# Performance work log

Hardware: AMD Instinct MI355X
Metric: run time of the kernel (lower is better)

Reference implementation:

```python
import jax, jax.numpy as jnp
import numpy as np

N_NODES = 100000
N_EDGES = 1600000
D = 64
K1 = 10   # conv1 hops
K2 = 3    # stacked conv hops


def _gcn_norm(edge_index, num_nodes, dtype):
    # PyG gcn_norm with add_self_loops=False: sym normalization D^-1/2 A D^-1/2
    row, col = edge_index[0], edge_index[1]
    deg = jax.ops.segment_sum(jnp.ones(row.shape, dtype), col, num_segments=num_nodes)
    dinv = jnp.where(deg > 0, jax.lax.rsqrt(jnp.maximum(deg, 1.0)), 0.0)
    return dinv[row] * dinv[col]  # [E]


def _tagconv(x, ws, b, row, col, nrm, num_nodes):
    # out = sum_k (A_hat^k x) @ W_k + b ; ws: [K+1, D, D]
    out = x @ ws[0]
    h = x
    for k in range(1, ws.shape[0]):
        msg = h[row] * nrm[:, None]                       # [E, D] gather
        h = jax.ops.segment_sum(msg, col, num_segments=num_nodes)  # [N, D] scatter-add
        out = out + h @ ws[k]
    return out + b


def setup_inputs() -> dict:
    key = jax.random.key(0)
    ks = jax.random.split(key, 8)
    x = jax.random.normal(ks[0], (N_NODES, D), dtype=jnp.float32)
    edge_index = jax.random.randint(ks[1], (2, N_EDGES), 0, N_NODES, dtype=jnp.int64)
    s = 1.0 / np.sqrt(D)
    w1 = jax.random.normal(ks[2], (K1 + 1, D, D), dtype=jnp.float32) * s
    b1 = jnp.zeros((D,), dtype=jnp.float32)
    w2 = jax.random.normal(ks[3], (K2 + 1, D, D), dtype=jnp.float32) * s
    b2 = jnp.zeros((D,), dtype=jnp.float32)
    wc = jax.random.normal(ks[4], (D, D), dtype=jnp.float32) * s
    bc = jnp.zeros((D,), dtype=jnp.float32)
    return {"x": x, "edge_index": edge_index, "w1": w1, "b1": b1,
            "w2": w2, "b2": b2, "wc": wc, "bc": bc}


def reference(x, edge_index, w1, b1, w2, b2, wc, bc):
    num_nodes = x.shape[0]
    row, col = edge_index[0], edge_index[1]
    nrm = _gcn_norm(edge_index, num_nodes, x.dtype)
    h = jnp.tanh(_tagconv(x, w1, b1, row, col, nrm, num_nodes))
    h = jnp.tanh(_tagconv(h, w2, b2, row, col, nrm, num_nodes))
    return h @ wc + bc
```

## Files before the change

kernel.cpp:

```cpp
#include <hip/hip_runtime.h>
#include <hip/hip_bf16.h>

#define PAD 16
#define NBKT_MAX 512

typedef __attribute__((ext_vector_type(8))) short short8;
typedef __attribute__((ext_vector_type(4))) float float4v;

__device__ __forceinline__ short8 as_s8(uint4 v) {
    union { uint4 u; short8 s; } x; x.u = v; return x.s;
}


__global__ void deg_kernel(const int* __restrict__ col, int* __restrict__ deg, int E) {
    int e = blockIdx.x * blockDim.x + threadIdx.x;
    if (e < E) atomicAdd(&deg[col[e]], 1);
}

__global__ void dinv_kernel(const int* __restrict__ deg, float* __restrict__ dinv,
                            float* __restrict__ dinv2, float* __restrict__ sdeg, int N) {
    int n = blockIdx.x * blockDim.x + threadIdx.x;
    if (n < N) {
        int d = deg[n];
        float v = d > 0 ? rsqrtf((float)d) : 0.0f;
        dinv[n] = v;
        dinv2[n] = v * v;
        sdeg[n] = d > 0 ? sqrtf((float)d) : 0.0f;
    }
}

__device__ __forceinline__ int pad_up(int v) { return (v + (PAD - 1)) & ~(PAD - 1); }

__global__ void scan_phaseA(const int* __restrict__ deg, int* __restrict__ chunkSum, int N) {
    int t = threadIdx.x;
    int idx = blockIdx.x * 512 + t;
    int v = idx < N ? pad_up(deg[idx]) : 0;
    for (int o = 32; o > 0; o >>= 1) v += __shfl_down(v, o, 64);
    __shared__ int wsum[8];
    if ((t & 63) == 0) wsum[t >> 6] = v;
    __syncthreads();
    if (t == 0) {
        int s = 0;
        for (int i = 0; i < 8; ++i) s += wsum[i];
        chunkSum[blockIdx.x] = s;
    }
}

__global__ void scan_phaseB(const int* __restrict__ in, int* __restrict__ outp, int n) {
    __shared__ int a[256], b[256];
    int t = threadIdx.x;
    int v = t < n ? in[t] : 0;
    a[t] = v;
    __syncthreads();
    int* s = a; int* d = b;
    for (int off = 1; off < 256; off <<= 1) {
        int x = s[t];
        if (t >= off) x += s[t - off];
        d[t] = x;
        __syncthreads();
        int* tmp = s; s = d; d = tmp;
    }
    if (t < n) outp[t] = s[t] - v;
}

__global__ void scan_phaseC(const int* __restrict__ deg, const int* __restrict__ chunkOff,
                            int* __restrict__ rowptr, int N) {
    __shared__ int a[512], b[512];
    int t = threadIdx.x;
    int idx = blockIdx.x * 512 + t;
    int v = idx < N ? pad_up(deg[idx]) : 0;
    a[t] = v;
    __syncthreads();
    int* s = a; int* d = b;
    for (int off = 1; off < 512; off <<= 1) {
        int x = s[t];
        if (t >= off) x += s[t - off];
        d[t] = x;
        __syncthreads();
        int* tmp = s; s = d; d = tmp;
    }
    if (idx < N) rowptr[idx] = chunkOff[blockIdx.x] + s[t] - v;
    if (idx == N - 1) rowptr[N] = chunkOff[blockIdx.x] + s[t];
}


__global__ __launch_bounds__(256) void hist_kernel(const int* __restrict__ col,
                                                   int* __restrict__ blockHist, int E, int nbkt) {
    __shared__ int h[NBKT_MAX];
    for (int i = threadIdx.x; i < nbkt; i += 256) h[i] = 0;
    __syncthreads();
    int chunk = (E + gridDim.x - 1) / gridDim.x;
    int lo = blockIdx.x * chunk, hi = min(lo + chunk, E);
    for (int e = lo + threadIdx.x; e < hi; e += 256) atomicAdd(&h[col[e] >> 9], 1);
    __syncthreads();
    for (int i = threadIdx.x; i < nbkt; i += 256) blockHist[i * 256 + blockIdx.x] = h[i];
}

__global__ __launch_bounds__(256) void bscan_kernel(int* __restrict__ blockHist,
                                                    int* __restrict__ bktTot, int nbkt) {
    __shared__ int a[256], b[256];
    int bkt = blockIdx.x;
    int t = threadIdx.x;
    int v = blockHist[bkt * 256 + t];
    a[t] = v;
    __syncthreads();
    int* s = a; int* d = b;
    for (int off = 1; off < 256; off <<= 1) {
        int x = s[t];
        if (t >= off) x += s[t - off];
        d[t] = x;
        __syncthreads();
        int* tmp = s; s = d; d = tmp;
    }
    blockHist[bkt * 256 + t] = s[t] - v;
    if (t == 255) bktTot[bkt] = s[t];
}

__global__ __launch_bounds__(256) void scatter_kernel(const int* __restrict__ row,
                                                      const int* __restrict__ col,
                                                      const int* __restrict__ blockHist,
                                                      const int* __restrict__ bktOff,
                                                      int2* __restrict__ pairs, int E, int nbkt) {
    __shared__ int cur[NBKT_MAX];
    for (int i = threadIdx.x; i < nbkt; i += 256)
        cur[i] = bktOff[i] + blockHist[i * 256 + blockIdx.x];
    __syncthreads();
    int chunk = (E + gridDim.x - 1) / gridDim.x;
    int lo = blockIdx.x * chunk, hi = min(lo + chunk, E);
    for (int e = lo + threadIdx.x; e < hi; e += 256) {
        int dn = col[e];
        int p = atomicAdd(&cur[dn >> 9], 1);
        pairs[p] = make_int2(row[e], dn);
    }
}

__global__ __launch_bounds__(256) void cluster_kernel(const int2* __restrict__ pairs,
                                                      const int* __restrict__ bktOff,
                                                      const int* __restrict__ bktTot,
                                                      const int* __restrict__ rowptr,
                                                      int* __restrict__ srcs, int N) {
    __shared__ int cur[512];
    int b = blockIdx.x;
    int d0 = b << 9;
    for (int i = threadIdx.x; i < 512; i += 256) {
        int d = d0 + i;
        cur[i] = (d < N) ? rowptr[d] : 0;
    }
    __syncthreads();
    int lo = bktOff[b], hi = lo + bktTot[b];
    for (int p = lo + threadIdx.x; p < hi; p += 256) {
        int2 e = pairs[p];
        int pos = atomicAdd(&cur[e.y - d0], 1);
        srcs[pos] = e.x;
    }
}

__global__ void pad_kernel(const int* __restrict__ deg, const int* __restrict__ rowptr,
                           int* __restrict__ srcs, int N) {
    int dn = blockIdx.x * blockDim.x + threadIdx.x;
    if (dn < N) {
        int p = rowptr[dn] + deg[dn];
        int p1 = rowptr[dn + 1];
        for (; p < p1; ++p) srcs[p] = N;
    }
}

__global__ void wcvt_kernel(const float* __restrict__ w1, const float* __restrict__ w2,
                            const float* __restrict__ wc, __hip_bfloat16* __restrict__ wf) {
    int idx = blockIdx.x * blockDim.x + threadIdx.x;
    if (idx >= 16 * 4096) return;
    int g = idx >> 12, r = idx & 4095;
    int j = r & 7, lane = (r >> 3) & 63, u = (r >> 9) & 3, t = r >> 11;
    int k = t * 32 + (lane >> 4) * 8 + j;
    int n = u * 16 + (lane & 15);
    const float* W = (g < 11) ? (w1 + (size_t)g * 4096)
                  : (g < 15) ? (w2 + (size_t)(g - 11) * 4096) : wc;
    wf[idx] = __float2bfloat16(W[k * 64 + n]);
}

__global__ void zero_pads_kernel(__hip_bfloat16* __restrict__ gbase, size_t gstride,
                                 int nbuf, int N) {
    int i = blockIdx.x * blockDim.x + threadIdx.x;
    int b = i >> 6;
    if (b < nbuf) gbase[(size_t)b * gstride + (size_t)N * 64 + (i & 63)] = __float2bfloat16(0.0f);
}

__global__ void cvt_g_kernel(const float* __restrict__ x, const float* __restrict__ dinv,
                             __hip_bfloat16* __restrict__ g, int N) {
    int i = blockIdx.x * blockDim.x + threadIdx.x;
    if (i < N * 64) g[i] = __float2bfloat16(dinv[i >> 6] * x[i]);
}


__global__ __launch_bounds__(256) void hop_kernel(
        const __hip_bfloat16* __restrict__ g_in,
        const int* __restrict__ srcs, const int* __restrict__ rowptr,
        const float* __restrict__ dinv2,
        __hip_bfloat16* __restrict__ g_out, int n) {
    const int lane = threadIdx.x & 63;
    int gw = __builtin_amdgcn_readfirstlane((blockIdx.x * blockDim.x + threadIdx.x) >> 6);
    int nw = (gridDim.x * blockDim.x) >> 6;
    for (int d = gw; d < n; d += nw) {
        int p0 = rowptr[d], p1 = rowptr[d + 1];
        float agg = 0.f;
        for (int p = p0; p < p1; p += 16) {
            int s0  = srcs[p + 0],  s1  = srcs[p + 1],  s2  = srcs[p + 2],  s3  = srcs[p + 3];
            int s4  = srcs[p + 4],  s5  = srcs[p + 5],  s6  = srcs[p + 6],  s7  = srcs[p + 7];
            int s8  = srcs[p + 8],  s9  = srcs[p + 9],  s10 = srcs[p + 10], s11 = srcs[p + 11];
            int s12 = srcs[p + 12], s13 = srcs[p + 13], s14 = srcs[p + 14], s15 = srcs[p + 15];
            float v0  = __bfloat162float(g_in[(size_t)s0  * 64 + lane]);
            float v1  = __bfloat162float(g_in[(size_t)s1  * 64 + lane]);
            float v2  = __bfloat162float(g_in[(size_t)s2  * 64 + lane]);
            float v3  = __bfloat162float(g_in[(size_t)s3  * 64 + lane]);
            float v4  = __bfloat162float(g_in[(size_t)s4  * 64 + lane]);
            float v5  = __bfloat162float(g_in[(size_t)s5  * 64 + lane]);
            float v6  = __bfloat162float(g_in[(size_t)s6  * 64 + lane]);
            float v7  = __bfloat162float(g_in[(size_t)s7  * 64 + lane]);
            float v8  = __bfloat162float(g_in[(size_t)s8  * 64 + lane]);
            float v9  = __bfloat162float(g_in[(size_t)s9  * 64 + lane]);
            float v10 = __bfloat162float(g_in[(size_t)s10 * 64 + lane]);
            float v11 = __bfloat162float(g_in[(size_t)s11 * 64 + lane]);
            float v12 = __bfloat162float(g_in[(size_t)s12 * 64 + lane]);
            float v13 = __bfloat162float(g_in[(size_t)s13 * 64 + lane]);
            float v14 = __bfloat162float(g_in[(size_t)s14 * 64 + lane]);
            float v15 = __bfloat162float(g_in[(size_t)s15 * 64 + lane]);
            agg += v0;  agg += v1;  agg += v2;  agg += v3;
            agg += v4;  agg += v5;  agg += v6;  agg += v7;
            agg += v8;  agg += v9;  agg += v10; agg += v11;
            agg += v12; agg += v13; agg += v14; agg += v15;
        }
        g_out[(size_t)d * 64 + lane] = __float2bfloat16(dinv2[d] * agg);
    }
}


__global__ __launch_bounds__(256) void final_kernel(
        const __hip_bfloat16* gbase, size_t gstride, int ngemm,
        const __hip_bfloat16* __restrict__ wf,
        const float* __restrict__ sdeg, const float* __restrict__ bias,
        const float* __restrict__ scale,
        __hip_bfloat16* out16, int ntiles) {
    const int lane = threadIdx.x & 63;
    const int col = lane & 15, quad = lane >> 4;
    int wv = (blockIdx.x * blockDim.x + threadIdx.x) >> 6;
    int nwv = (gridDim.x * blockDim.x) >> 6;
    const uint4* wfq = (const uint4*)wf;
    for (int tile = wv; tile < ntiles; tile += nwv) {
        int base = tile * 16;
        float4v acc0 = {0.f, 0.f, 0.f, 0.f};
        float4v acc1 = {0.f, 0.f, 0.f, 0.f};
        float4v acc2 = {0.f, 0.f, 0.f, 0.f};
        float4v acc3 = {0.f, 0.f, 0.f, 0.f};
        for (int g = 0; g < ngemm; ++g) {
            const uint4* ga = (const uint4*)(gbase + (size_t)g * gstride);
            const uint4* wg = wfq + (size_t)g * 512;
#pragma unroll
            for (int t = 0; t < 2; ++t) {
                short8 a = as_s8(ga[(size_t)(base + col) * 8 + t * 4 + quad]);
                short8 b0 = as_s8(wg[(t * 4 + 0) * 64 + lane]);
                short8 b1 = as_s8(wg[(t * 4 + 1) * 64 + lane]);
                short8 b2 = as_s8(wg[(t * 4 + 2) * 64 + lane]);
                short8 b3 = as_s8(wg[(t * 4 + 3) * 64 + lane]);
                acc0 = __builtin_amdgcn_mfma_f32_16x16x32_bf16(a, b0, acc0, 0, 0, 0);
                acc1 = __builtin_amdgcn_mfma_f32_16x16x32_bf16(a, b1, acc1, 0, 0, 0);
                acc2 = __builtin_amdgcn_mfma_f32_16x16x32_bf16(a, b2, acc2, 0, 0, 0);
                acc3 = __builtin_amdgcn_mfma_f32_16x16x32_bf16(a, b3, acc3, 0, 0, 0);
            }
        }
#pragma unroll
        for (int r = 0; r < 4; ++r) {
            int nd = base + quad * 4 + r;
            float sd = sdeg[nd];
            float sc = scale ? scale[nd] : 1.0f;
            float f0 = sc * tanhf(sd * acc0[r] + bias[0 * 16 + col]);
            float f1 = sc * tanhf(sd * acc1[r] + bias[1 * 16 + col]);
            float f2 = sc * tanhf(sd * acc2[r] + bias[2 * 16 + col]);
            float f3 = sc * tanhf(sd * acc3[r] + bias[3 * 16 + col]);
            out16[(size_t)nd * 64 + 0 * 16 + col] = __float2bfloat16(f0);
            out16[(size_t)nd * 64 + 1 * 16 + col] = __float2bfloat16(f1);
            out16[(size_t)nd * 64 + 2 * 16 + col] = __float2bfloat16(f2);
            out16[(size_t)nd * 64 + 3 * 16 + col] = __float2bfloat16(f3);
        }
    }
}


__global__ __launch_bounds__(256) void head_kernel(
        const __hip_bfloat16* __restrict__ v16, const __hip_bfloat16* __restrict__ wfc,
        const float* __restrict__ bc, float* __restrict__ out, int ntiles) {
    const int lane = threadIdx.x & 63;
    const int col = lane & 15, quad = lane >> 4;
    int wv = (blockIdx.x * blockDim.x + threadIdx.x) >> 6;
    int nwv = (gridDim.x * blockDim.x) >> 6;
    const uint4* va = (const uint4*)v16;
    const uint4* wg = (const uint4*)wfc;
    for (int tile = wv; tile < ntiles; tile += nwv) {
        int base = tile * 16;
        float4v acc0 = {0.f, 0.f, 0.f, 0.f};
        float4v acc1 = {0.f, 0.f, 0.f, 0.f};
        float4v acc2 = {0.f, 0.f, 0.f, 0.f};
        float4v acc3 = {0.f, 0.f, 0.f, 0.f};
#pragma unroll
        for (int t = 0; t < 2; ++t) {
            short8 a = as_s8(va[(size_t)(base + col) * 8 + t * 4 + quad]);
            short8 b0 = as_s8(wg[(t * 4 + 0) * 64 + lane]);
            short8 b1 = as_s8(wg[(t * 4 + 1) * 64 + lane]);
            short8 b2 = as_s8(wg[(t * 4 + 2) * 64 + lane]);
            short8 b3 = as_s8(wg[(t * 4 + 3) * 64 + lane]);
            acc0 = __builtin_amdgcn_mfma_f32_16x16x32_bf16(a, b0, acc0, 0, 0, 0);
            acc1 = __builtin_amdgcn_mfma_f32_16x16x32_bf16(a, b1, acc1, 0, 0, 0);
            acc2 = __builtin_amdgcn_mfma_f32_16x16x32_bf16(a, b2, acc2, 0, 0, 0);
            acc3 = __builtin_amdgcn_mfma_f32_16x16x32_bf16(a, b3, acc3, 0, 0, 0);
        }
#pragma unroll
        for (int r = 0; r < 4; ++r) {
            int nd = base + quad * 4 + r;
            out[(size_t)nd * 64 + 0 * 16 + col] = acc0[r] + bc[0 * 16 + col];
            out[(size_t)nd * 64 + 1 * 16 + col] = acc1[r] + bc[1 * 16 + col];
            out[(size_t)nd * 64 + 2 * 16 + col] = acc2[r] + bc[2 * 16 + col];
            out[(size_t)nd * 64 + 3 * 16 + col] = acc3[r] + bc[3 * 16 + col];
        }
    }
}


extern "C" void kernel_launch(void* const* d_in, const int* in_sizes, int n_in,
                              void* d_out, int out_size, void* d_ws, size_t ws_size,
                              hipStream_t stream) {
    const float* x  = (const float*)d_in[0];
    const int*   ei = (const int*)d_in[1];
    const float* w1 = (const float*)d_in[2];
    const float* b1 = (const float*)d_in[3];
    const float* w2 = (const float*)d_in[4];
    const float* b2 = (const float*)d_in[5];
    const float* wc = (const float*)d_in[6];
    const float* bc = (const float*)d_in[7];
    float* out = (float*)d_out;

    const int N = in_sizes[0] / 64;
    const int E = in_sizes[1] / 2;
    const int K1 = 10, K2 = 3;
    const int* row = ei;
    const int* col = ei + E;
    const int Epad = E + (PAD - 1) * N + 64;
    const int NBUF = 11;
    const int nbkt = (N + 511) >> 9;
    const size_t gstride = (((size_t)(N + 1) * 64) + 127) & ~(size_t)127;

    char* base = (char*)d_ws;
    auto alloc = [&](size_t bytes) { void* p = (void*)base; base += (bytes + 255) & ~(size_t)255; return p; };
    int*   deg      = (int*)alloc((size_t)N * 4);
    int*   rowptr   = (int*)alloc((size_t)(N + 1) * 4);
    int*   chunkSum = (int*)alloc(256 * 4);
    int*   chunkOff = (int*)alloc(256 * 4);
    int*   blockHist= (int*)alloc((size_t)NBKT_MAX * 256 * 4);
    int*   bktTot   = (int*)alloc((size_t)NBKT_MAX * 4);
    int*   bktOff   = (int*)alloc((size_t)NBKT_MAX * 4);
    float* dinv     = (float*)alloc((size_t)N * 4);
    float* dinv2    = (float*)alloc((size_t)N * 4);
    float* sdeg     = (float*)alloc((size_t)N * 4);
    int*   srcs     = (int*)alloc((size_t)Epad * 4);
    __hip_bfloat16* wf    = (__hip_bfloat16*)alloc((size_t)16 * 4096 * 2);
    __hip_bfloat16* gbase = (__hip_bfloat16*)alloc((size_t)NBUF * gstride * 2);

    auto G = [&](int k) { return gbase + (size_t)k * gstride; };
    int2* pairs = (int2*)G(9);
    __hip_bfloat16* vbuf16 = G(5);

    const int numChunks = (N + 511) / 512;
    const int eBlocks = (E + 255) / 256;
    const int nBlocks = (N + 255) / 256;
    const int xBlocks = (N * 64 + 255) / 256;
    const int gBlocks = 2048;
    const int ntiles = (N + 15) / 16;

    hipMemsetAsync(deg, 0, (size_t)N * 4, stream);
    deg_kernel<<<eBlocks, 256, 0, stream>>>(col, deg, E);
    dinv_kernel<<<nBlocks, 256, 0, stream>>>(deg, dinv, dinv2, sdeg, N);
    scan_phaseA<<<numChunks, 512, 0, stream>>>(deg, chunkSum, N);
    scan_phaseB<<<1, 256, 0, stream>>>(chunkSum, chunkOff, numChunks);
    scan_phaseC<<<numChunks, 512, 0, stream>>>(deg, chunkOff, rowptr, N);

    hist_kernel<<<256, 256, 0, stream>>>(col, blockHist, E, nbkt);
    bscan_kernel<<<nbkt, 256, 0, stream>>>(blockHist, bktTot, nbkt);
    scan_phaseB<<<1, 256, 0, stream>>>(bktTot, bktOff, nbkt);
    scatter_kernel<<<256, 256, 0, stream>>>(row, col, blockHist, bktOff, pairs, E, nbkt);
    cluster_kernel<<<nbkt, 256, 0, stream>>>(pairs, bktOff, bktTot, rowptr, srcs, N);
    pad_kernel<<<nBlocks, 256, 0, stream>>>(deg, rowptr, srcs, N);

    wcvt_kernel<<<(16 * 4096 + 255) / 256, 256, 0, stream>>>(w1, w2, wc, wf);
    zero_pads_kernel<<<(NBUF * 64 + 255) / 256, 256, 0, stream>>>(gbase, gstride, NBUF, N);
    cvt_g_kernel<<<xBlocks, 256, 0, stream>>>(x, dinv, G(0), N);

    for (int k = 1; k <= K1; ++k)
        hop_kernel<<<gBlocks, 256, 0, stream>>>(G(k - 1), srcs, rowptr, dinv2, G(k), N);

    final_kernel<<<gBlocks, 256, 0, stream>>>(gbase, gstride, 11, wf, sdeg, b1, dinv,
                                              G(1), ntiles);

    for (int k = 1; k <= K2; ++k)
        hop_kernel<<<gBlocks, 256, 0, stream>>>(G(k), srcs, rowptr, dinv2, G(k + 1), N);

    final_kernel<<<gBlocks, 256, 0, stream>>>(G(1), gstride, 4, wf + (size_t)11 * 4096,
                                              sdeg, b2, nullptr, vbuf16, ntiles);

    head_kernel<<<gBlocks, 256, 0, stream>>>(vbuf16, wf + (size_t)15 * 4096, bc, out, ntiles);
}
```

Measured before the change: 719.8 us.

## Compute degrees from bucketed pairs and fold padding into cluster kernel

Drops the global-atomic degree kernel and its memset. Degrees and the dinv/dinv2/sdeg values are now computed per 512-node bucket with shared-memory atomics over the already-bucketed edge pairs, and the CSR scan runs after the scatter. Padding of srcs with the sentinel moves into the tail of cluster_kernel using its final cursors, which removes the separate pad kernel. The aim is fewer launches and less contended global atomic traffic in preprocessing, at the cost of an extra pass over the pairs buffer.

```diff
diff --git a/kernel.cpp b/kernel.cpp
--- a/kernel.cpp
+++ b/kernel.cpp
@@ -11,45 +11,27 @@
     union { uint4 u; short8 s; } x; x.u = v; return x.s;
 }
 
-
-__global__ void deg_kernel(const int* __restrict__ col, int* __restrict__ deg, int E) {
-    int e = blockIdx.x * blockDim.x + threadIdx.x;
-    if (e < E) atomicAdd(&deg[col[e]], 1);
-}
-
-__global__ void dinv_kernel(const int* __restrict__ deg, float* __restrict__ dinv,
-                            float* __restrict__ dinv2, float* __restrict__ sdeg, int N) {
-    int n = blockIdx.x * blockDim.x + threadIdx.x;
-    if (n < N) {
-        int d = deg[n];
-        float v = d > 0 ? rsqrtf((float)d) : 0.0f;
-        dinv[n] = v;
-        dinv2[n] = v * v;
-        sdeg[n] = d > 0 ? sqrtf((float)d) : 0.0f;
-    }
-}
-
 __device__ __forceinline__ int pad_up(int v) { return (v + (PAD - 1)) & ~(PAD - 1); }
 
-__global__ void scan_phaseA(const int* __restrict__ deg, int* __restrict__ chunkSum, int N) {
+
+__global__ __launch_bounds__(256) void hist_kernel(const int* __restrict__ col,
+                                                   int* __restrict__ blockHist, int E, int nbkt) {
+    __shared__ int h[NBKT_MAX];
+    for (int i = threadIdx.x; i < nbkt; i += 256) h[i] = 0;
+    __syncthreads();
+    int chunk = (E + gridDim.x - 1) / gridDim.x;
+    int lo = blockIdx.x * chunk, hi = min(lo + chunk, E);
+    for (int e = lo + threadIdx.x; e < hi; e += 256) atomicAdd(&h[col[e] >> 9], 1);
+    __syncthreads();
+    for (int i = threadIdx.x; i < nbkt; i += 256) blockHist[i * 256 + blockIdx.x] = h[i];
+}
+
+__global__ __launch_bounds__(256) void bscan_kernel(int* __restrict__ blockHist,
+                                                    int* __restrict__ bktTot, int nbkt) {
+    __shared__ int a[256], b[256];
+    int bkt = blockIdx.x;
     int t = threadIdx.x;
-    int idx = blockIdx.x * 512 + t;
-    int v = idx < N ? pad_up(deg[idx]) : 0;
-    for (int o = 32; o > 0; o >>= 1) v += __shfl_down(v, o, 64);
-    __shared__ int wsum[8];
-    if ((t & 63) == 0) wsum[t >> 6] = v;
-    __syncthreads();
-    if (t == 0) {
-        int s = 0;
-        for (int i = 0; i < 8; ++i) s += wsum[i];
-        chunkSum[blockIdx.x] = s;
-    }
-}
-
-__global__ void scan_phaseB(const int* __restrict__ in, int* __restrict__ outp, int n) {
-    __shared__ int a[256], b[256];
-    int t = threadIdx.x;
-    int v = t < n ? in[t] : 0;
+    int v = blockHist[bkt * 256 + t];
     a[t] = v;
     __syncthreads();
     int* s = a; int* d = b;
@@ -60,48 +42,14 @@
         __syncthreads();
         int* tmp = s; s = d; d = tmp;
     }
-    if (t < n) outp[t] = s[t] - v;
-}
-
-__global__ void scan_phaseC(const int* __restrict__ deg, const int* __restrict__ chunkOff,
-                            int* __restrict__ rowptr, int N) {
-    __shared__ int a[512], b[512];
+    blockHist[bkt * 256 + t] = s[t] - v;
+    if (t == 255) bktTot[bkt] = s[t];
+}
+
+__global__ void scan_small(const int* __restrict__ in, int* __restrict__ outp, int n) {
+    __shared__ int a[256], b[256];
     int t = threadIdx.x;
-    int idx = blockIdx.x * 512 + t;
-    int v = idx < N ? pad_up(deg[idx]) : 0;
-    a[t] = v;
-    __syncthreads();
-    int* s = a; int* d = b;
-    for (int off = 1; off < 512; off <<= 1) {
-        int x = s[t];
-        if (t >= off) x += s[t - off];
-        d[t] = x;
-        __syncthreads();
-        int* tmp = s; s = d; d = tmp;
-    }
-    if (idx < N) rowptr[idx] = chunkOff[blockIdx.x] + s[t] - v;
-    if (idx == N - 1) rowptr[N] = chunkOff[blockIdx.x] + s[t];
-}
-
-
-__global__ __launch_bounds__(256) void hist_kernel(const int* __restrict__ col,
-                                                   int* __restrict__ blockHist, int E, int nbkt) {
-    __shared__ int h[NBKT_MAX];
-    for (int i = threadIdx.x; i < nbkt; i += 256) h[i] = 0;
-    __syncthreads();
-    int chunk = (E + gridDim.x - 1) / gridDim.x;
-    int lo = blockIdx.x * chunk, hi = min(lo + chunk, E);
-    for (int e = lo + threadIdx.x; e < hi; e += 256) atomicAdd(&h[col[e] >> 9], 1);
-    __syncthreads();
-    for (int i = threadIdx.x; i < nbkt; i += 256) blockHist[i * 256 + blockIdx.x] = h[i];
-}
-
-__global__ __launch_bounds__(256) void bscan_kernel(int* __restrict__ blockHist,
-                                                    int* __restrict__ bktTot, int nbkt) {
-    __shared__ int a[256], b[256];
-    int bkt = blockIdx.x;
-    int t = threadIdx.x;
-    int v = blockHist[bkt * 256 + t];
+    int v = t < n ? in[t] : 0;
     a[t] = v;
     __syncthreads();
     int* s = a; int* d = b;
@@ -112,8 +60,7 @@
         __syncthreads();
         int* tmp = s; s = d; d = tmp;
     }
-    blockHist[bkt * 256 + t] = s[t] - v;
-    if (t == 255) bktTot[bkt] = s[t];
+    if (t < n) outp[t] = s[t] - v;
 }
 
 __global__ __launch_bounds__(256) void scatter_kernel(const int* __restrict__ row,
@@ -132,6 +79,67 @@
         int p = atomicAdd(&cur[dn >> 9], 1);
         pairs[p] = make_int2(row[e], dn);
     }
+}
+
+__global__ __launch_bounds__(256) void deg_pairs_kernel(
+        const int2* __restrict__ pairs, const int* __restrict__ bktOff,
+        const int* __restrict__ bktTot,
+        int* __restrict__ deg, float* __restrict__ dinv, float* __restrict__ dinv2,
+        float* __restrict__ sdeg, int N) {
+    __shared__ int cnt[512];
+    int b = blockIdx.x, d0 = b << 9;
+    for (int i = threadIdx.x; i < 512; i += 256) cnt[i] = 0;
+    __syncthreads();
+    int lo = bktOff[b], hi = lo + bktTot[b];
+    for (int p = lo + threadIdx.x; p < hi; p += 256)
+        atomicAdd(&cnt[pairs[p].y - d0], 1);
+    __syncthreads();
+    for (int i = threadIdx.x; i < 512; i += 256) {
+        int d = d0 + i;
+        if (d < N) {
+            int c = cnt[i];
+            deg[d] = c;
+            float v = c > 0 ? rsqrtf((float)c) : 0.0f;
+            dinv[d] = v;
+            dinv2[d] = v * v;
+            sdeg[d] = c > 0 ? sqrtf((float)c) : 0.0f;
+        }
+    }
+}
+
+__global__ void scan_phaseA(const int* __restrict__ deg, int* __restrict__ chunkSum, int N) {
+    int t = threadIdx.x;
+    int idx = blockIdx.x * 512 + t;
+    int v = idx < N ? pad_up(deg[idx]) : 0;
+    for (int o = 32; o > 0; o >>= 1) v += __shfl_down(v, o, 64);
+    __shared__ int wsum[8];
+    if ((t & 63) == 0) wsum[t >> 6] = v;
+    __syncthreads();
+    if (t == 0) {
+        int s = 0;
+        for (int i = 0; i < 8; ++i) s += wsum[i];
+        chunkSum[blockIdx.x] = s;
+    }
+}
+
+__global__ void scan_phaseC(const int* __restrict__ deg, const int* __restrict__ chunkOff,
+                            int* __restrict__ rowptr, int N) {
+    __shared__ int a[512], b[512];
+    int t = threadIdx.x;
+    int idx = blockIdx.x * 512 + t;
+    int v = idx < N ? pad_up(deg[idx]) : 0;
+    a[t] = v;
+    __syncthreads();
+    int* s = a; int* d = b;
+    for (int off = 1; off < 512; off <<= 1) {
+        int x = s[t];
+        if (t >= off) x += s[t - off];
+        d[t] = x;
+        __syncthreads();
+        int* tmp = s; s = d; d = tmp;
+    }
+    if (idx < N) rowptr[idx] = chunkOff[blockIdx.x] + s[t] - v;
+    if (idx == N - 1) rowptr[N] = chunkOff[blockIdx.x] + s[t];
 }
 
 __global__ __launch_bounds__(256) void cluster_kernel(const int2* __restrict__ pairs,
@@ -153,17 +161,17 @@
         int pos = atomicAdd(&cur[e.y - d0], 1);
         srcs[pos] = e.x;
     }
-}
-
-__global__ void pad_kernel(const int* __restrict__ deg, const int* __restrict__ rowptr,
-                           int* __restrict__ srcs, int N) {
-    int dn = blockIdx.x * blockDim.x + threadIdx.x;
-    if (dn < N) {
-        int p = rowptr[dn] + deg[dn];
-        int p1 = rowptr[dn + 1];
-        for (; p < p1; ++p) srcs[p] = N;
-    }
-}
+    __syncthreads();
+    for (int i = threadIdx.x; i < 512; i += 256) {
+        int d = d0 + i;
+        if (d < N) {
+            int p = cur[i];
+            int p1 = rowptr[d + 1];
+            for (; p < p1; ++p) srcs[p] = N;
+        }
+    }
+}
+
 
 __global__ void wcvt_kernel(const float* __restrict__ w1, const float* __restrict__ w2,
                             const float* __restrict__ wc, __hip_bfloat16* __restrict__ wf) {
@@ -368,25 +376,20 @@
     __hip_bfloat16* vbuf16 = G(5);
 
     const int numChunks = (N + 511) / 512;
-    const int eBlocks = (E + 255) / 256;
     const int nBlocks = (N + 255) / 256;
     const int xBlocks = (N * 64 + 255) / 256;
     const int gBlocks = 2048;
     const int ntiles = (N + 15) / 16;
 
-    hipMemsetAsync(deg, 0, (size_t)N * 4, stream);
-    deg_kernel<<<eBlocks, 256, 0, stream>>>(col, deg, E);
-    dinv_kernel<<<nBlocks, 256, 0, stream>>>(deg, dinv, dinv2, sdeg, N);
-    scan_phaseA<<<numChunks, 512, 0, stream>>>(deg, chunkSum, N);
-    scan_phaseB<<<1, 256, 0, stream>>>(chunkSum, chunkOff, numChunks);
-    scan_phaseC<<<numChunks, 512, 0, stream>>>(deg, chunkOff, rowptr, N);
-
     hist_kernel<<<256, 256, 0, stream>>>(col, blockHist, E, nbkt);
     bscan_kernel<<<nbkt, 256, 0, stream>>>(blockHist, bktTot, nbkt);
-    scan_phaseB<<<1, 256, 0, stream>>>(bktTot, bktOff, nbkt);
+    scan_small<<<1, 256, 0, stream>>>(bktTot, bktOff, nbkt);
     scatter_kernel<<<256, 256, 0, stream>>>(row, col, blockHist, bktOff, pairs, E, nbkt);
+    deg_pairs_kernel<<<nbkt, 256, 0, stream>>>(pairs, bktOff, bktTot, deg, dinv, dinv2, sdeg, N);
+    scan_phaseA<<<numChunks, 512, 0, stream>>>(deg, chunkSum, N);
+    scan_small<<<1, 256, 0, stream>>>(chunkSum, chunkOff, numChunks);
+    scan_phaseC<<<numChunks, 512, 0, stream>>>(deg, chunkOff, rowptr, N);
     cluster_kernel<<<nbkt, 256, 0, stream>>>(pairs, bktOff, bktTot, rowptr, srcs, N);
-    pad_kernel<<<nBlocks, 256, 0, stream>>>(deg, rowptr, srcs, N);
 
     wcvt_kernel<<<(16 * 4096 + 255) / 256, 256, 0, stream>>>(w1, w2, wc, wf);
     zero_pads_kernel<<<(NBUF * 64 + 255) / 256, 256, 0, stream>>>(gbase, gstride, NBUF, N);
```

After: 657.6 us. -8.6%, faster.
